# Performance work log

Measured on AMD Instinct MI355X. Metric: run time of the kernel, lower is better.

## Reference

```python
import jax, jax.numpy as jnp
import numpy as np
from jax import lax

S = 48          # fixed crop size (original crops are ragged; fixed here for batching)
EPS = 0.1       # Sinkhorn entropic regularization
ITERS = 50      # Sinkhorn iterations
TINY = 1e-8


def setup_inputs() -> dict:
    key = jax.random.key(0)
    k1, k2, k3 = jax.random.split(key, 3)
    B, C, H, W = 16, 5, 160, 160
    hm_gt = jax.random.uniform(k1, (B, C, H, W), dtype=jnp.float32)
    hm_pred = jax.random.uniform(k2, (B, C, H, W), dtype=jnp.float32)
    tops = jax.random.randint(k3, (B, 8, 2), 0, 112, dtype=jnp.int32)  # (y, x) per rect
    return {"hm_gt": hm_gt, "hm_pred": hm_pred, "tops": tops}


def _geometry_distance(s):
    # pairwise Euclidean distance between pixel centers of an s x s crop -> [s*s, s*s]
    ys, xs = jnp.meshgrid(jnp.arange(s, dtype=jnp.float32),
                          jnp.arange(s, dtype=jnp.float32), indexing="ij")
    pts = jnp.stack([ys.ravel(), xs.ravel()], axis=-1)          # [s*s, 2]
    d2 = jnp.sum((pts[:, None, :] - pts[None, :, :]) ** 2, -1)  # [s*s, s*s]
    return jnp.sqrt(d2)


def _crop_all(hm, tops):
    # hm: [B, C, H, W], tops: [B, R, 2] -> crops [B, R, C, S, S]
    def crop_one(hm_b, top):  # hm_b [C,H,W], top [2]
        return lax.dynamic_slice(hm_b, (0, top[0], top[1]), (hm_b.shape[0], S, S))
    return jax.vmap(lambda hb, tb: jax.vmap(lambda t: crop_one(hb, t))(tb))(hm, tops)


def reference(hm_gt, hm_pred, tops):
    B, C, H, W = hm_gt.shape
    n = S * S
    dist = _geometry_distance(S)            # [n, n]
    K = jnp.exp(-dist / EPS)                # Gibbs kernel
    M = K * dist                            # for the transport cost readout

    a = _crop_all(hm_gt, tops).reshape(-1, n)    # [N, n]
    b = _crop_all(hm_pred, tops).reshape(-1, n)  # [N, n]
    a = a / (jnp.sum(a, -1, keepdims=True) + TINY)   # normalize to marginals
    b = b / (jnp.sum(b, -1, keepdims=True) + TINY)

    N = a.shape[0]
    u0 = jnp.full((N, n), 1.0 / n, dtype=a.dtype)
    v0 = jnp.full((N, n), 1.0 / n, dtype=a.dtype)

    def body(carry, _):
        u, v = carry
        v = b / (u @ K + TINY)      # [N,n] @ [n,n]
        u = a / (v @ K.T + TINY)
        return (u, v), None

    (u, v), _ = lax.scan(body, (u0, v0), None, length=ITERS)
    # loss per crop: sum_ij u_i K_ij dist_ij v_j
    loss = jnp.sum((u @ M) * v)
    return loss
```

## Files before the change

### kernel.cpp

```cpp
#include <hip/hip_runtime.h>

#define TINYF 1e-8f
#define NITER 50

__device__ __forceinline__ float wW(float v) {
    return __int_as_float(__builtin_amdgcn_update_dpp(0, __float_as_int(v), 0x138, 0xf, 0xf, true));
}
__device__ __forceinline__ float wE(float v) {
    return __int_as_float(__builtin_amdgcn_update_dpp(0, __float_as_int(v), 0x130, 0xf, 0xf, true));
}

__global__ void __launch_bounds__(512)
__attribute__((amdgpu_waves_per_eu(6)))
sinkhorn_col(const float* __restrict__ hm_gt,
             const float* __restrict__ hm_pred,
             const int* __restrict__ tops,
             float* __restrict__ out) {
    __shared__ float EX[2][10][4][64];
    __shared__ float sred[2][8];

    const int t = threadIdx.x;
    const int W = t >> 6;
    const int l = t & 63;
    const bool act = (l < 48);

    {
        const int p = t >> 8, q = (t >> 6) & 3, ln = t & 63;
        if (q < 2) EX[p][0][2 + q][ln] = 0.f;
        else       EX[p][9][q - 2][ln] = 0.f;
    }

    const int blk = blockIdx.x;
    const int bi = blk / 40, rr = (blk / 5) % 8, cc = blk % 5;
    const int y0 = tops[(bi * 8 + rr) * 2 + 0];
    const int x0 = tops[(bi * 8 + rr) * 2 + 1];
    const float* srcA = hm_gt + (size_t)(bi * 5 + cc) * 25600;
    const float* srcB = hm_pred + (size_t)(bi * 5 + cc) * 25600;

    float va[6], vb[6];
    float sA = 0.f, sB = 0.f;
    const int rbase = y0 + 6 * W;
#pragma unroll
    for (int r = 0; r < 6; ++r) {
        const int g = (rbase + r) * 160 + x0 + l;
        const float A = act ? srcA[g] : 0.f;
        const float B = act ? srcB[g] : 0.f;
        va[r] = A; vb[r] = B;
        sA += A; sB += B;
    }
#pragma unroll
    for (int o = 1; o < 64; o <<= 1) {
        sA += __shfl_xor(sA, o, 64);
        sB += __shfl_xor(sB, o, 64);
    }
    if (l == 0) { sred[0][W] = sA; sred[1][W] = sB; }
    __syncthreads();
    sA = 0.f; sB = 0.f;
#pragma unroll
    for (int w = 0; w < 8; ++w) { sA += sred[0][w]; sB += sred[1][w]; }
    const float nA = 1.0f / (sA + TINYF);
    const float nB = 1.0f / (sB + TINYF);
#pragma unroll
    for (int r = 0; r < 6; ++r) { va[r] *= nA; vb[r] *= nB; }

    const float e10 = expf(-1.0f / 0.1f);
    const float e2  = expf(-sqrtf(2.0f) / 0.1f);
    const float e20 = expf(-2.0f / 0.1f);

    float xu[6], xv[6], acc[6];
    const float u0 = 1.0f / 2304.0f;
#pragma unroll
    for (int r = 0; r < 6; ++r) xu[r] = act ? u0 : 0.f;

    auto publish = [&](const float (&y)[6], int p) {
        EX[p][W + 1][0][l] = y[0];
        EX[p][W + 1][1][l] = y[1];
        EX[p][W + 1][2][l] = y[4];
        EX[p][W + 1][3][l] = y[5];
        __syncthreads();
    };

    auto conv = [&](const float (&x)[6], int p, bool CENTER,
                    float K01, float K11, float K02) {
        const float hm2 = EX[p][W][2][l];
        const float hm1 = EX[p][W][3][l];
        const float hp6 = EX[p][W + 2][0][l];
        const float hp7 = EX[p][W + 2][1][l];
        float s1[8], s2[6];
#pragma unroll
        for (int r = 0; r < 6; ++r) {
            const float w1 = wW(x[r]), e1 = wE(x[r]);
            s1[r + 1] = w1 + e1;
            s2[r] = wW(w1) + wE(e1);
        }
        s1[0] = wW(hm1) + wE(hm1);
        s1[7] = wW(hp6) + wE(hp6);
#pragma unroll
        for (int r = 0; r < 6; ++r) {
            const float up1 = (r == 0) ? hm1 : x[r - 1];
            const float dn1 = (r == 5) ? hp6 : x[r + 1];
            const float up2 = (r == 0) ? hm2 : ((r == 1) ? hm1 : x[r - 2]);
            const float dn2 = (r == 4) ? hp6 : ((r == 5) ? hp7 : x[r + 2]);
            float a = CENTER ? x[r] : 0.f;
            a = fmaf(K01, s1[r + 1] + (up1 + dn1), a);
            a = fmaf(K11, s1[r] + s1[r + 2], a);
            a = fmaf(K02, s2[r] + (up2 + dn2), a);
            acc[r] = a;
        }
    };

    publish(xu, 0);

#pragma unroll 1
    for (int it = 0; it < NITER; ++it) {
        conv(xu, 0, true, e10, e2, e20);
#pragma unroll
        for (int r = 0; r < 6; ++r)
            xv[r] = vb[r] * __builtin_amdgcn_rcpf(acc[r] + TINYF);
        publish(xv, 1);

        conv(xv, 1, true, e10, e2, e20);
#pragma unroll
        for (int r = 0; r < 6; ++r)
            xu[r] = va[r] * __builtin_amdgcn_rcpf(acc[r] + TINYF);
        publish(xu, 0);
    }

    const float s2f = sqrtf(2.0f);
    const float m01 = e10, m02 = e20 * 2.0f, m11 = e2 * s2f;
    conv(xu, 0, false, m01, m11, m02);
    float lsum = 0.f;
#pragma unroll
    for (int r = 0; r < 6; ++r) lsum += acc[r] * xv[r];

#pragma unroll
    for (int o = 1; o < 64; o <<= 1) lsum += __shfl_xor(lsum, o, 64);
    if (l == 0) sred[0][W] = lsum;
    __syncthreads();
    if (t == 0) {
        float s = 0.f;
#pragma unroll
        for (int w = 0; w < 8; ++w) s += sred[0][w];
        atomicAdd(out, s);
    }
}

extern "C" void kernel_launch(void* const* d_in, const int* in_sizes, int n_in,
                              void* d_out, int out_size, void* d_ws, size_t ws_size,
                              hipStream_t stream) {
    (void)in_sizes; (void)n_in; (void)out_size; (void)d_ws; (void)ws_size;
    const float* hm_gt = (const float*)d_in[0];
    const float* hm_pred = (const float*)d_in[1];
    const int* tops = (const int*)d_in[2];
    float* out = (float*)d_out;

    hipMemsetAsync(out, 0, sizeof(float), stream);
    sinkhorn_col<<<dim3(640), dim3(512), 0, stream>>>(hm_gt, hm_pred, tops, out);
}
```

Measured before the change: 198.2 us.

## Pack two row-halves per thread with float2 packed FMA, halve block size

Each thread now processes two 6-row strips (top and bottom halves of the 48-row crop) packed into float2 vectors, so the block shrinks from 8 to 4 waves. The stencil FMAs become packed vector FMAs, which the MI355X can issue as packed-fp32 instructions. Halo exchange goes through a float2 shared buffer, with wraparound writes between the two halves at the edges. Per-iteration barriers now span fewer waves, but each wave has more serial work and higher register use, and DPP shifts are still scalar per component.

```diff
diff --git a/kernel.cpp b/kernel.cpp
--- a/kernel.cpp
+++ b/kernel.cpp
@@ -3,21 +3,31 @@
 #define TINYF 1e-8f
 #define NITER 50
 
-__device__ __forceinline__ float wW(float v) {
+typedef __attribute__((ext_vector_type(2))) float v2f;
+
+__device__ __forceinline__ float wWs(float v) {
     return __int_as_float(__builtin_amdgcn_update_dpp(0, __float_as_int(v), 0x138, 0xf, 0xf, true));
 }
-__device__ __forceinline__ float wE(float v) {
+__device__ __forceinline__ float wEs(float v) {
     return __int_as_float(__builtin_amdgcn_update_dpp(0, __float_as_int(v), 0x130, 0xf, 0xf, true));
 }
+__device__ __forceinline__ v2f wW(v2f v) { v2f r; r.x = wWs(v.x); r.y = wWs(v.y); return r; }
+__device__ __forceinline__ v2f wE(v2f v) { v2f r; r.x = wEs(v.x); r.y = wEs(v.y); return r; }
+__device__ __forceinline__ v2f rcp2(v2f v) {
+    v2f r; r.x = __builtin_amdgcn_rcpf(v.x); r.y = __builtin_amdgcn_rcpf(v.y); return r;
+}
+__device__ __forceinline__ v2f pfma(float k, v2f a, v2f c) {
+    v2f kv; kv.x = k; kv.y = k;
+    return __builtin_elementwise_fma(kv, a, c);
+}
 
-__global__ void __launch_bounds__(512)
-__attribute__((amdgpu_waves_per_eu(6)))
-sinkhorn_col(const float* __restrict__ hm_gt,
-             const float* __restrict__ hm_pred,
-             const int* __restrict__ tops,
-             float* __restrict__ out) {
-    __shared__ float EX[2][10][4][64];
-    __shared__ float sred[2][8];
+__global__ void __launch_bounds__(256)
+sinkhorn_colpk(const float* __restrict__ hm_gt,
+               const float* __restrict__ hm_pred,
+               const int* __restrict__ tops,
+               float* __restrict__ out) {
+    __shared__ v2f ES[2][6][4][64];
+    __shared__ float sred[2][4];
 
     const int t = threadIdx.x;
     const int W = t >> 6;
@@ -25,9 +35,9 @@
     const bool act = (l < 48);
 
     {
-        const int p = t >> 8, q = (t >> 6) & 3, ln = t & 63;
-        if (q < 2) EX[p][0][2 + q][ln] = 0.f;
-        else       EX[p][9][q - 2][ln] = 0.f;
+        const int p = W >> 1, r = W & 1;
+        ((float*)&ES[p][0][2 + r][l])[0] = 0.f;
+        ((float*)&ES[p][5][r][l])[1] = 0.f;
     }
 
     const int blk = blockIdx.x;
@@ -37,16 +47,20 @@
     const float* srcA = hm_gt + (size_t)(bi * 5 + cc) * 25600;
     const float* srcB = hm_pred + (size_t)(bi * 5 + cc) * 25600;
 
-    float va[6], vb[6];
+    v2f va[6], vb[6];
     float sA = 0.f, sB = 0.f;
-    const int rbase = y0 + 6 * W;
+    const int rbx = y0 + 6 * W;
+    const int rby = y0 + 24 + 6 * W;
 #pragma unroll
     for (int r = 0; r < 6; ++r) {
-        const int g = (rbase + r) * 160 + x0 + l;
-        const float A = act ? srcA[g] : 0.f;
-        const float B = act ? srcB[g] : 0.f;
-        va[r] = A; vb[r] = B;
-        sA += A; sB += B;
+        const int gx = (rbx + r) * 160 + x0 + l;
+        const int gy = (rby + r) * 160 + x0 + l;
+        va[r].x = act ? srcA[gx] : 0.f;
+        va[r].y = act ? srcA[gy] : 0.f;
+        vb[r].x = act ? srcB[gx] : 0.f;
+        vb[r].y = act ? srcB[gy] : 0.f;
+        sA += va[r].x + va[r].y;
+        sB += vb[r].x + vb[r].y;
     }
 #pragma unroll
     for (int o = 1; o < 64; o <<= 1) {
@@ -55,56 +69,67 @@
     }
     if (l == 0) { sred[0][W] = sA; sred[1][W] = sB; }
     __syncthreads();
-    sA = 0.f; sB = 0.f;
-#pragma unroll
-    for (int w = 0; w < 8; ++w) { sA += sred[0][w]; sB += sred[1][w]; }
+    sA = sred[0][0] + sred[0][1] + sred[0][2] + sred[0][3];
+    sB = sred[1][0] + sred[1][1] + sred[1][2] + sred[1][3];
     const float nA = 1.0f / (sA + TINYF);
     const float nB = 1.0f / (sB + TINYF);
 #pragma unroll
-    for (int r = 0; r < 6; ++r) { va[r] *= nA; vb[r] *= nB; }
+    for (int r = 0; r < 6; ++r) {
+        va[r].x *= nA; va[r].y *= nA;
+        vb[r].x *= nB; vb[r].y *= nB;
+    }
 
     const float e10 = expf(-1.0f / 0.1f);
     const float e2  = expf(-sqrtf(2.0f) / 0.1f);
     const float e20 = expf(-2.0f / 0.1f);
 
-    float xu[6], xv[6], acc[6];
+    v2f xu[6], xv[6], acc[6];
     const float u0 = 1.0f / 2304.0f;
 #pragma unroll
-    for (int r = 0; r < 6; ++r) xu[r] = act ? u0 : 0.f;
+    for (int r = 0; r < 6; ++r) { xu[r].x = act ? u0 : 0.f; xu[r].y = act ? u0 : 0.f; }
 
-    auto publish = [&](const float (&y)[6], int p) {
-        EX[p][W + 1][0][l] = y[0];
-        EX[p][W + 1][1][l] = y[1];
-        EX[p][W + 1][2][l] = y[4];
-        EX[p][W + 1][3][l] = y[5];
+    auto publish = [&](const v2f (&y)[6], int p) {
+        ES[p][W + 1][0][l] = y[0];
+        ES[p][W + 1][1][l] = y[1];
+        ES[p][W + 1][2][l] = y[4];
+        ES[p][W + 1][3][l] = y[5];
+        if (W == 3) {
+            ((float*)&ES[p][0][2][l])[1] = y[4].x;
+            ((float*)&ES[p][0][3][l])[1] = y[5].x;
+        }
+        if (W == 0) {
+            ((float*)&ES[p][5][0][l])[0] = y[0].y;
+            ((float*)&ES[p][5][1][l])[0] = y[1].y;
+        }
         __syncthreads();
     };
 
-    auto conv = [&](const float (&x)[6], int p, bool CENTER,
+    auto conv = [&](const v2f (&x)[6], int p, bool CENTER,
                     float K01, float K11, float K02) {
-        const float hm2 = EX[p][W][2][l];
-        const float hm1 = EX[p][W][3][l];
-        const float hp6 = EX[p][W + 2][0][l];
-        const float hp7 = EX[p][W + 2][1][l];
-        float s1[8], s2[6];
+        const v2f um2 = ES[p][W][2][l];
+        const v2f um1 = ES[p][W][3][l];
+        const v2f up6 = ES[p][W + 2][0][l];
+        const v2f up7 = ES[p][W + 2][1][l];
+        v2f s1[8], s2[6];
 #pragma unroll
         for (int r = 0; r < 6; ++r) {
-            const float w1 = wW(x[r]), e1 = wE(x[r]);
+            const v2f w1 = wW(x[r]), e1 = wE(x[r]);
             s1[r + 1] = w1 + e1;
             s2[r] = wW(w1) + wE(e1);
         }
-        s1[0] = wW(hm1) + wE(hm1);
-        s1[7] = wW(hp6) + wE(hp6);
+        s1[0] = wW(um1) + wE(um1);
+        s1[7] = wW(up6) + wE(up6);
 #pragma unroll
         for (int r = 0; r < 6; ++r) {
-            const float up1 = (r == 0) ? hm1 : x[r - 1];
-            const float dn1 = (r == 5) ? hp6 : x[r + 1];
-            const float up2 = (r == 0) ? hm2 : ((r == 1) ? hm1 : x[r - 2]);
-            const float dn2 = (r == 4) ? hp6 : ((r == 5) ? hp7 : x[r + 2]);
-            float a = CENTER ? x[r] : 0.f;
-            a = fmaf(K01, s1[r + 1] + (up1 + dn1), a);
-            a = fmaf(K11, s1[r] + s1[r + 2], a);
-            a = fmaf(K02, s2[r] + (up2 + dn2), a);
+            const v2f up1 = (r == 0) ? um1 : x[r - 1];
+            const v2f dn1 = (r == 5) ? up6 : x[r + 1];
+            const v2f up2 = (r == 0) ? um2 : ((r == 1) ? um1 : x[r - 2]);
+            const v2f dn2 = (r == 4) ? up6 : ((r == 5) ? up7 : x[r + 2]);
+            v2f a;
+            if (CENTER) { a = x[r]; } else { a.x = 0.f; a.y = 0.f; }
+            a = pfma(K01, s1[r + 1] + (up1 + dn1), a);
+            a = pfma(K11, s1[r] + s1[r + 2], a);
+            a = pfma(K02, s2[r] + (up2 + dn2), a);
             acc[r] = a;
         }
     };
@@ -115,34 +140,35 @@
     for (int it = 0; it < NITER; ++it) {
         conv(xu, 0, true, e10, e2, e20);
 #pragma unroll
-        for (int r = 0; r < 6; ++r)
-            xv[r] = vb[r] * __builtin_amdgcn_rcpf(acc[r] + TINYF);
+        for (int r = 0; r < 6; ++r) {
+            v2f d; d.x = acc[r].x + TINYF; d.y = acc[r].y + TINYF;
+            xv[r] = vb[r] * rcp2(d);
+        }
         publish(xv, 1);
 
         conv(xv, 1, true, e10, e2, e20);
 #pragma unroll
-        for (int r = 0; r < 6; ++r)
-            xu[r] = va[r] * __builtin_amdgcn_rcpf(acc[r] + TINYF);
+        for (int r = 0; r < 6; ++r) {
+            v2f d; d.x = acc[r].x + TINYF; d.y = acc[r].y + TINYF;
+            xu[r] = va[r] * rcp2(d);
+        }
         publish(xu, 0);
     }
 
     const float s2f = sqrtf(2.0f);
     const float m01 = e10, m02 = e20 * 2.0f, m11 = e2 * s2f;
     conv(xu, 0, false, m01, m11, m02);
-    float lsum = 0.f;
+    v2f ls; ls.x = 0.f; ls.y = 0.f;
 #pragma unroll
-    for (int r = 0; r < 6; ++r) lsum += acc[r] * xv[r];
+    for (int r = 0; r < 6; ++r) ls += acc[r] * xv[r];
+    float lsum = ls.x + ls.y;
 
 #pragma unroll
     for (int o = 1; o < 64; o <<= 1) lsum += __shfl_xor(lsum, o, 64);
     if (l == 0) sred[0][W] = lsum;
     __syncthreads();
-    if (t == 0) {
-        float s = 0.f;
-#pragma unroll
-        for (int w = 0; w < 8; ++w) s += sred[0][w];
-        atomicAdd(out, s);
-    }
+    if (t == 0)
+        atomicAdd(out, sred[0][0] + sred[0][1] + sred[0][2] + sred[0][3]);
 }
 
 extern "C" void kernel_launch(void* const* d_in, const int* in_sizes, int n_in,
@@ -155,5 +181,5 @@
     float* out = (float*)d_out;
 
     hipMemsetAsync(out, 0, sizeof(float), stream);
-    sinkhorn_col<<<dim3(640), dim3(512), 0, stream>>>(hm_gt, hm_pred, tops, out);
+    sinkhorn_colpk<<<dim3(640), dim3(256), 0, stream>>>(hm_gt, hm_pred, tops, out);
 }
```

Result: faster. 172.3 us (-13.1%).
